# Kernel tuning notes

Hardware: AMD Instinct MI355X
Metric: run time of the kernel (lower is better)

Reference implementation:

```python
import math
import jax, jax.numpy as jnp
import numpy as np

V, D, L, H, B, T = 50257, 1024, 6, 16, 4, 1024
HD = D // H  # 64


def layer_norm(x, s, b, eps=1e-5):
    m = jnp.mean(x, axis=-1, keepdims=True)
    v = jnp.var(x, axis=-1, keepdims=True)
    return (x - m) * jax.lax.rsqrt(v + eps) * s + b


def setup_inputs() -> dict:
    key = jax.random.key(0)
    ks = jax.random.split(key, 8)
    sc = 0.02
    return {
        "input_ids": jax.random.randint(ks[0], (B, T), 0, V),
        "attention_mask": jnp.ones((B, T), jnp.float32),
        "pool_mask": jax.random.uniform(ks[1], (B, T), dtype=jnp.float32),
        "embed": jax.random.normal(ks[2], (V, D), jnp.float32) * sc,
        "ln1_s": jnp.ones((L, D), jnp.float32),
        "ln1_b": jnp.zeros((L, D), jnp.float32),
        "qkv_w": jax.random.normal(ks[3], (L, D, 3 * D), jnp.float32) * sc,
        "qkv_b": jnp.zeros((L, 3 * D), jnp.float32),
        "attn_w": jax.random.normal(ks[4], (L, D, D), jnp.float32) * sc,
        "attn_b": jnp.zeros((L, D), jnp.float32),
        "ln2_s": jnp.ones((L, D), jnp.float32),
        "ln2_b": jnp.zeros((L, D), jnp.float32),
        "fc1_w": jax.random.normal(ks[5], (L, D, 4 * D), jnp.float32) * sc,
        "fc1_b": jnp.zeros((L, 4 * D), jnp.float32),
        "fc2_w": jax.random.normal(ks[6], (L, 4 * D, D), jnp.float32) * sc,
        "fc2_b": jnp.zeros((L, D), jnp.float32),
    }


def reference(input_ids, attention_mask, pool_mask, embed, ln1_s, ln1_b,
              qkv_w, qkv_b, attn_w, attn_b, ln2_s, ln2_b,
              fc1_w, fc1_b, fc2_w, fc2_b):
    h = embed[input_ids]  # [B,T,D]
    # key_mask.clamp(min=0) then log(clamp(min=1e-9)) == log(clip(mask, 1e-9))
    log_mask = jnp.log(jnp.clip(attention_mask, 1e-9))[:, None, None, :]  # [B,1,1,T]
    scale = 1.0 / math.sqrt(HD)

    def block(h, p):
        l1s, l1b, qw, qb, aw, ab, l2s, l2b, f1w, f1b, f2w, f2b = p
        x = layer_norm(h, l1s, l1b)
        qkv = jnp.einsum('btd,de->bte', x, qw) + qb          # [B,T,3D]
        qkv = qkv.reshape(B, T, H, 3 * HD).transpose(0, 2, 1, 3)  # [B,H,T,3hd]
        q, k, v = jnp.split(qkv, 3, axis=-1)
        scores = jnp.einsum('bhqd,bhkd->bhqk', q, k) * scale + log_mask
        probs = jax.nn.softmax(scores, axis=-1)
        ctx = jnp.einsum('bhqk,bhkd->bhqd', probs, v)
        ctx = ctx.transpose(0, 2, 1, 3).reshape(B, T, D)
        h = h + jnp.einsum('btd,de->bte', ctx, aw) + ab
        y = layer_norm(h, l2s, l2b)
        y = jax.nn.gelu(jnp.einsum('btd,df->btf', y, f1w) + f1b, approximate=False)
        h = h + jnp.einsum('btf,fd->btd', y, f2w) + f2b
        # NOTE: source applies post_attention_layernorm a second time at block end
        h = layer_norm(h, l2s, l2b)
        return h, None

    params = (ln1_s, ln1_b, qkv_w, qkv_b, attn_w, attn_b,
              ln2_s, ln2_b, fc1_w, fc1_b, fc2_w, fc2_b)
    h, _ = jax.lax.scan(block, h, params)

    # pool with pool_mask, then L2-normalize (F.normalize, eps=1e-12)
    m = pool_mask[..., None]
    sent = (h * m).sum(axis=1) / jnp.clip(m.sum(axis=1), 1e-6)
    return sent / jnp.clip(jnp.linalg.norm(sent, axis=-1, keepdims=True), 1e-12)
```

## Files before the change

kernel.cpp:

```cpp
#include <hip/hip_runtime.h>
#include <hip/hip_bf16.h>
#include <math.h>

#define VV 50257
#define DD 1024
#define LL 6
#define HH 16
#define BB 4
#define TT 1024
#define HD 64
#define BT (BB*TT)

typedef __attribute__((ext_vector_type(8))) short bf16x8;
typedef __attribute__((ext_vector_type(8))) _Float16 f16x8;
typedef __attribute__((ext_vector_type(4))) short short4v;
typedef __attribute__((ext_vector_type(4))) float f32x4;
typedef __attribute__((ext_vector_type(16))) float f32x16;

__device__ inline float b2f(unsigned short u) {
    unsigned x = ((unsigned)u) << 16;
    return __uint_as_float(x);
}
__device__ inline unsigned short f2b(float f) {
    __hip_bfloat16 h = __float2bfloat16(f);
    return *reinterpret_cast<unsigned short*>(&h);
}
__device__ inline void plswap32(unsigned &dst, unsigned &src) {
    asm("v_permlane32_swap_b32 %0, %1" : "+v"(dst), "+v"(src));
}

#define GLOAD16(g, l) __builtin_amdgcn_global_load_lds( \
    (const __attribute__((address_space(1))) void*)(g), \
    (__attribute__((address_space(3))) void*)(l), 16, 0, 0)

__launch_bounds__(256)
__global__ void gather_embed(const int* __restrict__ ids, const float* __restrict__ emb,
                             float* __restrict__ h) {
    const int row = blockIdx.x;
    const int id = ids[row];
    const float4* src = (const float4*)(emb + (size_t)id * DD);
    float4* dst = (float4*)(h + (size_t)row * DD);
    dst[threadIdx.x] = src[threadIdx.x];
}

__launch_bounds__(256)
__global__ void logmask_k(const float* __restrict__ am, float* __restrict__ lm) {
    int i = blockIdx.x * 256 + threadIdx.x;
    if (i < BT) lm[i] = logf(fmaxf(am[i], 1e-9f));
}

__device__ inline float block_sum_256(float v, float* ws) {
    #pragma unroll
    for (int o = 32; o > 0; o >>= 1) v += __shfl_down(v, o);
    const int lane = threadIdx.x & 63, wid = threadIdx.x >> 6;
    if (lane == 0) ws[wid] = v;
    __syncthreads();
    return ws[0] + ws[1] + ws[2] + ws[3];
}

__launch_bounds__(256)
__global__ void ln_f32(const float* __restrict__ in, float* __restrict__ out,
                       const float* __restrict__ g, const float* __restrict__ bta) {
    __shared__ float ws1[4], ws2[4];
    const int row = blockIdx.x, tid = threadIdx.x;
    const float* x = in + (size_t)row * DD;
    float4 v = *(const float4*)(x + tid * 4);
    float s = v.x + v.y + v.z + v.w;
    float tot = block_sum_256(s, ws1);
    float m = tot * (1.0f / 1024.0f);
    float d0 = v.x - m, d1 = v.y - m, d2 = v.z - m, d3 = v.w - m;
    float s2 = d0*d0 + d1*d1 + d2*d2 + d3*d3;
    float tot2 = block_sum_256(s2, ws2);
    float rstd = rsqrtf(tot2 * (1.0f / 1024.0f) + 1e-5f);
    const int d = tid * 4;
    float4 gg = *(const float4*)(g + d);
    float4 bb = *(const float4*)(bta + d);
    float4 o;
    o.x = d0 * rstd * gg.x + bb.x;
    o.y = d1 * rstd * gg.y + bb.y;
    o.z = d2 * rstd * gg.z + bb.z;
    o.w = d3 * rstd * gg.w + bb.w;
    *(float4*)(out + (size_t)row * DD + d) = o;
}

__launch_bounds__(256)
__global__ void ln_bf16(const float* __restrict__ in, unsigned short* __restrict__ out,
                        const float* __restrict__ g, const float* __restrict__ bta) {
    __shared__ float ws1[4], ws2[4];
    const int row = blockIdx.x, tid = threadIdx.x;
    const float* x = in + (size_t)row * DD;
    float4 v = *(const float4*)(x + tid * 4);
    float s = v.x + v.y + v.z + v.w;
    float tot = block_sum_256(s, ws1);
    float m = tot * (1.0f / 1024.0f);
    float d0 = v.x - m, d1 = v.y - m, d2 = v.z - m, d3 = v.w - m;
    float s2 = d0*d0 + d1*d1 + d2*d2 + d3*d3;
    float tot2 = block_sum_256(s2, ws2);
    float rstd = rsqrtf(tot2 * (1.0f / 1024.0f) + 1e-5f);
    const int d = tid * 4;
    float4 gg = *(const float4*)(g + d);
    float4 bb = *(const float4*)(bta + d);
    ushort4 o;
    o.x = f2b(d0 * rstd * gg.x + bb.x);
    o.y = f2b(d1 * rstd * gg.y + bb.y);
    o.z = f2b(d2 * rstd * gg.z + bb.z);
    o.w = f2b(d3 * rstd * gg.w + bb.w);
    *(ushort4*)(out + (size_t)row * DD + d) = o;
}

__launch_bounds__(256)
__global__ void wtrans(const float* __restrict__ W, unsigned short* __restrict__ Wt,
                       int K, int N) {
    __shared__ float tile[64][65];
    const int k0 = blockIdx.y * 64, n0 = blockIdx.x * 64;
    const int lrow = threadIdx.x >> 4;
    const int lcol = (threadIdx.x & 15) * 4;
    #pragma unroll
    for (int i = 0; i < 4; ++i) {
        const int r = lrow + i * 16;
        *(float4*)&tile[r][lcol] = *(const float4*)(W + (size_t)(k0 + r) * N + n0 + lcol);
    }
    __syncthreads();
    #pragma unroll
    for (int i = 0; i < 4; ++i) {
        const int n = lrow + i * 16;
        ushort4 o;
        o.x = f2b(tile[lcol + 0][n]);
        o.y = f2b(tile[lcol + 1][n]);
        o.z = f2b(tile[lcol + 2][n]);
        o.w = f2b(tile[lcol + 3][n]);
        *(ushort4*)(Wt + (size_t)(n0 + n) * K + k0 + lcol) = o;
    }
}

#define BM 128
#define BN 128
#define BK 64

__device__ inline float gelu_f(float v) {
    return 0.5f * v * (1.0f + erff(v * 0.70710678118654752f));
}

template<int EPI>
__launch_bounds__(256)
__global__ void gemm_mfma(const unsigned short* __restrict__ A,
                          const unsigned short* __restrict__ Bt,
                          const float* __restrict__ bias, void* __restrict__ Cv,
                          int M, int K, int N) {
    __shared__ short As[BM * BK];
    __shared__ short Bs[BN * BK];

    const int tid = threadIdx.x;
    const int wid = tid >> 6, lane = tid & 63;

    const int nwg = gridDim.x * gridDim.y;
    int bid = blockIdx.y * gridDim.x + blockIdx.x;
    bid = (bid & 7) * (nwg >> 3) + (bid >> 3);
    const int m0 = (bid / gridDim.x) * BM;
    const int n0 = (bid % gridDim.x) * BN;

    const int wr = wid >> 1, wc = wid & 1;
    const int fr = lane & 15, fq = lane >> 4;

    const int rowS = tid >> 3;
    const int cS = tid & 7;
    const int coff = (cS ^ (rowS & 7)) * 8;
    const unsigned short* aS = A  + (size_t)(m0 + rowS) * K + coff;
    const unsigned short* bS = Bt + (size_t)(n0 + rowS) * K + coff;
    const size_t rstride = (size_t)32 * K;

    const int key = fr & 7;
    const int c0 = fq ^ key;
    int aoff[4], boff[4];
    #pragma unroll
    for (int m = 0; m < 4; ++m) aoff[m] = (wr * 64 + m * 16 + fr) * BK + c0 * 8;
    #pragma unroll
    for (int n = 0; n < 4; ++n) boff[n] = (wc * 64 + n * 16 + fr) * BK + c0 * 8;

    f32x4 acc[4][4];
    #pragma unroll
    for (int m = 0; m < 4; ++m)
        #pragma unroll
        for (int n = 0; n < 4; ++n) acc[m][n] = (f32x4){0.f, 0.f, 0.f, 0.f};

    for (int kk = 0; kk < K; kk += BK) {
        __syncthreads();
        #pragma unroll
        for (int r = 0; r < 4; ++r) {
            GLOAD16(aS + kk + r * rstride, &As[(wid * 64 + r * 256) * 8]);
            GLOAD16(bS + kk + r * rstride, &Bs[(wid * 64 + r * 256) * 8]);
        }
        __syncthreads();
        #pragma unroll
        for (int s = 0; s < 2; ++s) {
            bf16x8 af[4], bfr[4];
            #pragma unroll
            for (int m = 0; m < 4; ++m) af[m] = *(const bf16x8*)&As[aoff[m] ^ (s << 5)];
            #pragma unroll
            for (int n = 0; n < 4; ++n) bfr[n] = *(const bf16x8*)&Bs[boff[n] ^ (s << 5)];
            #pragma unroll
            for (int m = 0; m < 4; ++m)
                #pragma unroll
                for (int n = 0; n < 4; ++n)
                    acc[m][n] = __builtin_amdgcn_mfma_f32_16x16x32_bf16(
                        af[m], bfr[n], acc[m][n], 0, 0, 0);
        }
    }

    float bias_v[4];
    #pragma unroll
    for (int n = 0; n < 4; ++n) bias_v[n] = bias[n0 + wc * 64 + n * 16 + fr];

    #pragma unroll
    for (int m = 0; m < 4; ++m) {
        #pragma unroll
        for (int n = 0; n < 4; ++n) {
            const int col = n0 + wc * 64 + n * 16 + fr;
            #pragma unroll
            for (int j = 0; j < 4; ++j) {
                const int row = m0 + wr * 64 + m * 16 + fq * 4 + j;
                float v = acc[m][n][j] + bias_v[n];
                if (EPI == 1) {
                    float* C = (float*)Cv;
                    C[(size_t)row * N + col] += v;
                } else {
                    if (EPI == 2) v = gelu_f(v);
                    unsigned short* C = (unsigned short*)Cv;
                    C[(size_t)row * N + col] = f2b(v);
                }
            }
        }
    }
}

__launch_bounds__(256)
__global__ void attn_mfma(const unsigned short* __restrict__ qkv,
                          const float* __restrict__ lm,
                          unsigned short* __restrict__ ctx) {
    int bid = blockIdx.x;
    const int ww = (bid & 7) * 64 + (bid >> 3);
    const int bh = ww >> 3, qt = ww & 7;
    const int b = bh >> 4, hh = bh & 15;
    const int tid = threadIdx.x, w = tid >> 6, lane = tid & 63;
    const int lo = lane & 31, hf = lane >> 5;
    const int q_row = qt * 128 + w * 32 + lo;

    __shared__ short Ks[32 * 64];
    __shared__ short Vt[64 * 40];
    __shared__ float lms[32];

    bf16x8 qf[4];
    {
        const unsigned short* qbase = qkv + (size_t)(b * TT + q_row) * 3072 + hh * 192;
        #pragma unroll
        for (int kk = 0; kk < 4; ++kk)
            qf[kk] = *(const bf16x8*)(qbase + (2 * kk + hf) * 8);
    }

    const int skey = tid >> 3, sc = tid & 7;
    const unsigned short* kptr = qkv + (size_t)(b * TT + skey) * 3072 + hh * 192 + 64
                                 + ((sc ^ (skey & 7)) * 8);
    short* kdst = &Ks[w * 64 * 8];

    const int vkey = tid & 31, vc = tid >> 5;
    const unsigned short* vptr = qkv + (size_t)(b * TT + vkey) * 3072 + hh * 192 + 128 + vc * 8;

    f32x16 o0, o1;
    #pragma unroll
    for (int j = 0; j < 16; ++j) { o0[j] = 0.f; o1[j] = 0.f; }
    float M = -1e30f, S = 0.f;

    for (int kt = 0; kt < 32; ++kt) {
        __syncthreads();
        GLOAD16(kptr, kdst);
        bf16x8 vv = *(const bf16x8*)vptr;
        if (tid < 32) lms[tid] = lm[b * TT + kt * 32 + tid];
        #pragma unroll
        for (int i = 0; i < 8; ++i) {
            _Float16 hv = (_Float16)b2f((unsigned short)vv[i]);
            Vt[(vc * 8 + i) * 40 + vkey] = *reinterpret_cast<short*>(&hv);
        }
        kptr += (size_t)32 * 3072;
        vptr += (size_t)32 * 3072;
        __syncthreads();

        f32x16 s16;
        #pragma unroll
        for (int j = 0; j < 16; ++j) s16[j] = 0.f;
        __builtin_amdgcn_s_setprio(1);
        #pragma unroll
        for (int kk = 0; kk < 4; ++kk) {
            const int c = (2 * kk + hf) ^ (lo & 7);
            bf16x8 kf = *(const bf16x8*)&Ks[lo * 64 + c * 8];
            s16 = __builtin_amdgcn_mfma_f32_32x32x16_bf16(kf, qf[kk], s16, 0, 0, 0);
        }
        __builtin_amdgcn_s_setprio(0);

        float p[16];
        float mx = -1e30f;
        #pragma unroll
        for (int j = 0; j < 16; ++j) {
            const int kidx = (j & 3) + 8 * (j >> 2) + 4 * hf;
            float sv = s16[j] * 0.125f + lms[kidx];
            p[j] = sv;
            mx = fmaxf(mx, sv);
        }
        mx = fmaxf(mx, __shfl_xor(mx, 32));
        if (!__all(mx <= M + 8.0f)) {
            const float Mn = fmaxf(M, mx);
            const float f = __expf(M - Mn);
            S *= f;
            #pragma unroll
            for (int j = 0; j < 16; ++j) { o0[j] *= f; o1[j] *= f; }
            M = Mn;
        }

        unsigned short ph[16];
        float ls = 0.f;
        #pragma unroll
        for (int j = 0; j < 16; ++j) {
            _Float16 hq = (_Float16)__expf(p[j] - M);
            ph[j] = *reinterpret_cast<unsigned short*>(&hq);
            ls += (float)hq;
        }
        ls += __shfl_xor(ls, 32);
        S += ls;

        unsigned ra = (unsigned)ph[0]  | ((unsigned)ph[1]  << 16);
        unsigned rb = (unsigned)ph[2]  | ((unsigned)ph[3]  << 16);
        unsigned rc = (unsigned)ph[4]  | ((unsigned)ph[5]  << 16);
        unsigned rd = (unsigned)ph[6]  | ((unsigned)ph[7]  << 16);
        unsigned re = (unsigned)ph[8]  | ((unsigned)ph[9]  << 16);
        unsigned rf = (unsigned)ph[10] | ((unsigned)ph[11] << 16);
        unsigned rg = (unsigned)ph[12] | ((unsigned)ph[13] << 16);
        unsigned rh = (unsigned)ph[14] | ((unsigned)ph[15] << 16);
        plswap32(ra, rc);
        plswap32(rb, rd);
        plswap32(re, rg);
        plswap32(rf, rh);
        union { unsigned u[4]; f16x8 v; } p1, p2;
        p1.u[0] = ra; p1.u[1] = rb; p1.u[2] = rc; p1.u[3] = rd;
        p2.u[0] = re; p2.u[1] = rf; p2.u[2] = rg; p2.u[3] = rh;

        f16x8 va0 = *(const f16x8*)&Vt[lo * 40 + hf * 8];
        f16x8 va1 = *(const f16x8*)&Vt[lo * 40 + 16 + hf * 8];
        f16x8 vb0 = *(const f16x8*)&Vt[(32 + lo) * 40 + hf * 8];
        f16x8 vb1 = *(const f16x8*)&Vt[(32 + lo) * 40 + 16 + hf * 8];
        __builtin_amdgcn_s_setprio(1);
        o0 = __builtin_amdgcn_mfma_f32_32x32x16_f16(va0, p1.v, o0, 0, 0, 0);
        o0 = __builtin_amdgcn_mfma_f32_32x32x16_f16(va1, p2.v, o0, 0, 0, 0);
        o1 = __builtin_amdgcn_mfma_f32_32x32x16_f16(vb0, p1.v, o1, 0, 0, 0);
        o1 = __builtin_amdgcn_mfma_f32_32x32x16_f16(vb1, p2.v, o1, 0, 0, 0);
        __builtin_amdgcn_s_setprio(0);
    }

    const float inv = 1.f / S;
    unsigned short* obase = ctx + (size_t)(b * TT + q_row) * DD + hh * 64;
    #pragma unroll
    for (int g = 0; g < 4; ++g) {
        const int dbase = 8 * g + 4 * hf;
        ushort4 w0, w1;
        w0.x = f2b(o0[4*g+0] * inv); w0.y = f2b(o0[4*g+1] * inv);
        w0.z = f2b(o0[4*g+2] * inv); w0.w = f2b(o0[4*g+3] * inv);
        w1.x = f2b(o1[4*g+0] * inv); w1.y = f2b(o1[4*g+1] * inv);
        w1.z = f2b(o1[4*g+2] * inv); w1.w = f2b(o1[4*g+3] * inv);
        *(ushort4*)(obase + dbase) = w0;
        *(ushort4*)(obase + 32 + dbase) = w1;
    }
}

__launch_bounds__(256)
__global__ void pool_partial(const float* __restrict__ h, const float* __restrict__ pm,
                             float* __restrict__ part) {
    const int b = blockIdx.x >> 4, c = blockIdx.x & 15;
    const int tid = threadIdx.x;
    const float* hp = h + (size_t)(b * TT + c * 64) * DD + tid * 4;
    const float* pp = pm + b * TT + c * 64;
    float4 acc = {0.f, 0.f, 0.f, 0.f};
    for (int t = 0; t < 64; ++t) {
        const float p = pp[t];
        float4 v = *(const float4*)(hp + (size_t)t * DD);
        acc.x += p * v.x; acc.y += p * v.y; acc.z += p * v.z; acc.w += p * v.w;
    }
    *(float4*)(part + (size_t)blockIdx.x * DD + tid * 4) = acc;
}

__launch_bounds__(1024)
__global__ void pool_final(const float* __restrict__ part, const float* __restrict__ pm,
                           float* __restrict__ out) {
    const int b = blockIdx.x, d = threadIdx.x;
    __shared__ float ws[16];
    float s = pm[b * TT + d];
    #pragma unroll
    for (int o = 32; o > 0; o >>= 1) s += __shfl_down(s, o);
    if ((d & 63) == 0) ws[d >> 6] = s;
    __syncthreads();
    float msum = 0.f;
    #pragma unroll
    for (int i = 0; i < 16; ++i) msum += ws[i];

    float acc = 0.f;
    #pragma unroll
    for (int c = 0; c < 16; ++c)
        acc += part[(size_t)(b * 16 + c) * DD + d];
    const float sent = acc / fmaxf(msum, 1e-6f);

    float qv = sent * sent;
    #pragma unroll
    for (int o = 32; o > 0; o >>= 1) qv += __shfl_down(qv, o);
    __syncthreads();
    if ((d & 63) == 0) ws[d >> 6] = qv;
    __syncthreads();
    float nrm = 0.f;
    #pragma unroll
    for (int i = 0; i < 16; ++i) nrm += ws[i];
    nrm = sqrtf(nrm);
    out[b * DD + d] = sent / fmaxf(nrm, 1e-12f);
}

extern "C" void kernel_launch(void* const* d_in, const int* in_sizes, int n_in,
                              void* d_out, int out_size, void* d_ws, size_t ws_size,
                              hipStream_t stream) {
    const int*   ids    = (const int*)  d_in[0];
    const float* amask  = (const float*)d_in[1];
    const float* pmask  = (const float*)d_in[2];
    const float* embed  = (const float*)d_in[3];
    const float* ln1_s  = (const float*)d_in[4];
    const float* ln1_b  = (const float*)d_in[5];
    const float* qkv_w  = (const float*)d_in[6];
    const float* qkv_b  = (const float*)d_in[7];
    const float* attn_w = (const float*)d_in[8];
    const float* attn_b = (const float*)d_in[9];
    const float* ln2_s  = (const float*)d_in[10];
    const float* ln2_b  = (const float*)d_in[11];
    const float* fc1_w  = (const float*)d_in[12];
    const float* fc1_b  = (const float*)d_in[13];
    const float* fc2_w  = (const float*)d_in[14];
    const float* fc2_b  = (const float*)d_in[15];

    char* wp = (char*)d_ws;
    float* h = (float*)wp;                 wp += (size_t)BT * DD * 4;
    unsigned short* qkv_bf = (unsigned short*)wp; wp += (size_t)BT * 3072 * 2;
    unsigned short* act_bf = (unsigned short*)wp; wp += (size_t)BT * 4096 * 2;
    unsigned short* x_bf   = (unsigned short*)wp; wp += (size_t)BT * DD * 2;
    unsigned short* wq_t   = (unsigned short*)wp; wp += (size_t)3072 * 1024 * 2;
    unsigned short* wa_t   = (unsigned short*)wp; wp += (size_t)1024 * 1024 * 2;
    unsigned short* w1_t   = (unsigned short*)wp; wp += (size_t)4096 * 1024 * 2;
    unsigned short* w2_t   = (unsigned short*)wp; wp += (size_t)1024 * 4096 * 2;
    float* lm = (float*)wp;                wp += (size_t)BT * 4;
    float* part = (float*)wp;              wp += (size_t)64 * DD * 4;

    gather_embed<<<BT, 256, 0, stream>>>(ids, embed, h);
    logmask_k<<<16, 256, 0, stream>>>(amask, lm);

    for (int l = 0; l < LL; ++l) {
        const size_t lD = (size_t)l * DD;

        wtrans<<<dim3(3072/64, 1024/64), 256, 0, stream>>>(
            qkv_w + (size_t)l * 1024 * 3072, wq_t, 1024, 3072);
        wtrans<<<dim3(1024/64, 1024/64), 256, 0, stream>>>(
            attn_w + (size_t)l * 1024 * 1024, wa_t, 1024, 1024);
        wtrans<<<dim3(4096/64, 1024/64), 256, 0, stream>>>(
            fc1_w + (size_t)l * 1024 * 4096, w1_t, 1024, 4096);
        wtrans<<<dim3(1024/64, 4096/64), 256, 0, stream>>>(
            fc2_w + (size_t)l * 4096 * 1024, w2_t, 4096, 1024);

        ln_bf16<<<BT, 256, 0, stream>>>(h, x_bf, ln1_s + lD, ln1_b + lD);
        gemm_mfma<0><<<dim3(3072/BN, BT/BM), 256, 0, stream>>>(
            x_bf, wq_t, qkv_b + (size_t)l * 3072, qkv_bf, BT, 1024, 3072);
        attn_mfma<<<512, 256, 0, stream>>>(qkv_bf, lm, x_bf);
        gemm_mfma<1><<<dim3(1024/BN, BT/BM), 256, 0, stream>>>(
            x_bf, wa_t, attn_b + lD, h, BT, 1024, 1024);
        ln_bf16<<<BT, 256, 0, stream>>>(h, x_bf, ln2_s + lD, ln2_b + lD);
        gemm_mfma<2><<<dim3(4096/BN, BT/BM), 256, 0, stream>>>(
            x_bf, w1_t, fc1_b + (size_t)l * 4096, act_bf, BT, 1024, 4096);
        gemm_mfma<1><<<dim3(1024/BN, BT/BM), 256, 0, stream>>>(
            act_bf, w2_t, fc2_b + lD, h, BT, 4096, 1024);
        ln_f32<<<BT, 256, 0, stream>>>(h, h, ln2_s + lD, ln2_b + lD);
    }

    pool_partial<<<64, 256, 0, stream>>>(h, pmask, part);
    pool_final<<<BB, 1024, 0, stream>>>(part, pmask, (float*)d_out);
}
```

Before: 1.870 ms.

## Fuse layernorms and weight transposes, narrow N-tiles, double-buffer attention K/V

Fuses the end-of-block layernorm with the next layer's first layernorm into one kernel, and merges the four weight-transpose launches into a single launch. The GEMM is templated on N-fragments so the N=1024 GEMMs use 64-wide tiles and launch more workgroups. The attention kernel now processes 64-key tiles with double-buffered K/V in shared memory, loading the next tile while computing the current one. These changes target launch overhead, low occupancy on the narrow GEMMs, and load latency in attention, at the cost of more shared memory per attention block and more code.

```diff
diff --git a/kernel.cpp b/kernel.cpp
--- a/kernel.cpp
+++ b/kernel.cpp
@@ -13,7 +13,6 @@
 
 typedef __attribute__((ext_vector_type(8))) short bf16x8;
 typedef __attribute__((ext_vector_type(8))) _Float16 f16x8;
-typedef __attribute__((ext_vector_type(4))) short short4v;
 typedef __attribute__((ext_vector_type(4))) float f32x4;
 typedef __attribute__((ext_vector_type(16))) float f32x16;
 
@@ -109,10 +108,55 @@
 }
 
 __launch_bounds__(256)
-__global__ void wtrans(const float* __restrict__ W, unsigned short* __restrict__ Wt,
-                       int K, int N) {
+__global__ void ln_dual(const float* __restrict__ in, float* __restrict__ outf,
+                        const float* __restrict__ g2, const float* __restrict__ b2v,
+                        unsigned short* __restrict__ outb,
+                        const float* __restrict__ g1, const float* __restrict__ b1v) {
+    __shared__ float ws1[4], ws2[4], ws3[4], ws4[4];
+    const int row = blockIdx.x, tid = threadIdx.x;
+    const int d = tid * 4;
+    float4 v = *(const float4*)(in + (size_t)row * DD + d);
+    float s = v.x + v.y + v.z + v.w;
+    float m = block_sum_256(s, ws1) * (1.0f / 1024.0f);
+    float d0 = v.x - m, d1 = v.y - m, d2 = v.z - m, d3 = v.w - m;
+    float s2 = d0*d0 + d1*d1 + d2*d2 + d3*d3;
+    float rstd = rsqrtf(block_sum_256(s2, ws2) * (1.0f / 1024.0f) + 1e-5f);
+    float4 gg = *(const float4*)(g2 + d);
+    float4 bb = *(const float4*)(b2v + d);
+    float4 y;
+    y.x = d0 * rstd * gg.x + bb.x;
+    y.y = d1 * rstd * gg.y + bb.y;
+    y.z = d2 * rstd * gg.z + bb.z;
+    y.w = d3 * rstd * gg.w + bb.w;
+    *(float4*)(outf + (size_t)row * DD + d) = y;
+    float t = y.x + y.y + y.z + y.w;
+    float m2 = block_sum_256(t, ws3) * (1.0f / 1024.0f);
+    float e0 = y.x - m2, e1 = y.y - m2, e2 = y.z - m2, e3 = y.w - m2;
+    float t2 = e0*e0 + e1*e1 + e2*e2 + e3*e3;
+    float rstd2 = rsqrtf(block_sum_256(t2, ws4) * (1.0f / 1024.0f) + 1e-5f);
+    float4 g1v = *(const float4*)(g1 + d);
+    float4 b1x = *(const float4*)(b1v + d);
+    ushort4 o;
+    o.x = f2b(e0 * rstd2 * g1v.x + b1x.x);
+    o.y = f2b(e1 * rstd2 * g1v.y + b1x.y);
+    o.z = f2b(e2 * rstd2 * g1v.z + b1x.z);
+    o.w = f2b(e3 * rstd2 * g1v.w + b1x.w);
+    *(ushort4*)(outb + (size_t)row * DD + d) = o;
+}
+
+__launch_bounds__(256)
+__global__ void wtrans4(const float* __restrict__ wq, unsigned short* __restrict__ wqo,
+                        const float* __restrict__ wa, unsigned short* __restrict__ wao,
+                        const float* __restrict__ w1, unsigned short* __restrict__ w1o,
+                        const float* __restrict__ w2, unsigned short* __restrict__ w2o) {
     __shared__ float tile[64][65];
-    const int k0 = blockIdx.y * 64, n0 = blockIdx.x * 64;
+    int id = blockIdx.x;
+    const float* W; unsigned short* Wt; int K, N, tx, ty;
+    if (id < 768)       { W = wq; Wt = wqo; K = 1024; N = 3072; tx = id % 48; ty = id / 48; }
+    else if (id < 1024) { id -= 768;  W = wa; Wt = wao; K = 1024; N = 1024; tx = id & 15; ty = id >> 4; }
+    else if (id < 2048) { id -= 1024; W = w1; Wt = w1o; K = 1024; N = 4096; tx = id & 63; ty = id >> 6; }
+    else                { id -= 2048; W = w2; Wt = w2o; K = 4096; N = 1024; tx = id & 15; ty = id >> 4; }
+    const int k0 = ty * 64, n0 = tx * 64;
     const int lrow = threadIdx.x >> 4;
     const int lcol = (threadIdx.x & 15) * 4;
     #pragma unroll
@@ -134,19 +178,19 @@
 }
 
 #define BM 128
-#define BN 128
 #define BK 64
 
 __device__ inline float gelu_f(float v) {
     return 0.5f * v * (1.0f + erff(v * 0.70710678118654752f));
 }
 
-template<int EPI>
+template<int EPI, int NFRAG>
 __launch_bounds__(256)
 __global__ void gemm_mfma(const unsigned short* __restrict__ A,
                           const unsigned short* __restrict__ Bt,
                           const float* __restrict__ bias, void* __restrict__ Cv,
                           int M, int K, int N) {
+    constexpr int BN = NFRAG * 32;
     __shared__ short As[BM * BK];
     __shared__ short Bs[BN * BK];
 
@@ -171,51 +215,52 @@
 
     const int key = fr & 7;
     const int c0 = fq ^ key;
-    int aoff[4], boff[4];
+    int aoff[4], boff[NFRAG];
     #pragma unroll
     for (int m = 0; m < 4; ++m) aoff[m] = (wr * 64 + m * 16 + fr) * BK + c0 * 8;
     #pragma unroll
-    for (int n = 0; n < 4; ++n) boff[n] = (wc * 64 + n * 16 + fr) * BK + c0 * 8;
-
-    f32x4 acc[4][4];
+    for (int n = 0; n < NFRAG; ++n) boff[n] = (wc * (NFRAG * 16) + n * 16 + fr) * BK + c0 * 8;
+
+    f32x4 acc[4][NFRAG];
     #pragma unroll
     for (int m = 0; m < 4; ++m)
         #pragma unroll
-        for (int n = 0; n < 4; ++n) acc[m][n] = (f32x4){0.f, 0.f, 0.f, 0.f};
+        for (int n = 0; n < NFRAG; ++n) acc[m][n] = (f32x4){0.f, 0.f, 0.f, 0.f};
 
     for (int kk = 0; kk < K; kk += BK) {
         __syncthreads();
         #pragma unroll
-        for (int r = 0; r < 4; ++r) {
+        for (int r = 0; r < 4; ++r)
             GLOAD16(aS + kk + r * rstride, &As[(wid * 64 + r * 256) * 8]);
+        #pragma unroll
+        for (int r = 0; r < NFRAG; ++r)
             GLOAD16(bS + kk + r * rstride, &Bs[(wid * 64 + r * 256) * 8]);
-        }
         __syncthreads();
         #pragma unroll
         for (int s = 0; s < 2; ++s) {
-            bf16x8 af[4], bfr[4];
+            bf16x8 af[4], bfr[NFRAG];
             #pragma unroll
             for (int m = 0; m < 4; ++m) af[m] = *(const bf16x8*)&As[aoff[m] ^ (s << 5)];
             #pragma unroll
-            for (int n = 0; n < 4; ++n) bfr[n] = *(const bf16x8*)&Bs[boff[n] ^ (s << 5)];
+            for (int n = 0; n < NFRAG; ++n) bfr[n] = *(const bf16x8*)&Bs[boff[n] ^ (s << 5)];
             #pragma unroll
             for (int m = 0; m < 4; ++m)
                 #pragma unroll
-                for (int n = 0; n < 4; ++n)
+                for (int n = 0; n < NFRAG; ++n)
                     acc[m][n] = __builtin_amdgcn_mfma_f32_16x16x32_bf16(
                         af[m], bfr[n], acc[m][n], 0, 0, 0);
         }
     }
 
-    float bias_v[4];
-    #pragma unroll
-    for (int n = 0; n < 4; ++n) bias_v[n] = bias[n0 + wc * 64 + n * 16 + fr];
+    float bias_v[NFRAG];
+    #pragma unroll
+    for (int n = 0; n < NFRAG; ++n) bias_v[n] = bias[n0 + wc * (NFRAG * 16) + n * 16 + fr];
 
     #pragma unroll
     for (int m = 0; m < 4; ++m) {
         #pragma unroll
-        for (int n = 0; n < 4; ++n) {
-            const int col = n0 + wc * 64 + n * 16 + fr;
+        for (int n = 0; n < NFRAG; ++n) {
+            const int col = n0 + wc * (NFRAG * 16) + n * 16 + fr;
             #pragma unroll
             for (int j = 0; j < 4; ++j) {
                 const int row = m0 + wr * 64 + m * 16 + fq * 4 + j;
@@ -245,9 +290,9 @@
     const int lo = lane & 31, hf = lane >> 5;
     const int q_row = qt * 128 + w * 32 + lo;
 
-    __shared__ short Ks[32 * 64];
-    __shared__ short Vt[64 * 40];
-    __shared__ float lms[32];
+    __shared__ short Ks[2][64 * 64];
+    __shared__ short Vt[2][64 * 72];
+    __shared__ float lms[2][64];
 
     bf16x8 qf[4];
     {
@@ -257,101 +302,125 @@
             qf[kk] = *(const bf16x8*)(qbase + (2 * kk + hf) * 8);
     }
 
-    const int skey = tid >> 3, sc = tid & 7;
-    const unsigned short* kptr = qkv + (size_t)(b * TT + skey) * 3072 + hh * 192 + 64
-                                 + ((sc ^ (skey & 7)) * 8);
-    short* kdst = &Ks[w * 64 * 8];
-
+    const int r0 = tid >> 3, cS = tid & 7;
+    const unsigned short* kp = qkv + (size_t)(b * TT + r0) * 3072 + hh * 192 + 64
+                               + ((cS ^ (r0 & 7)) * 8);
     const int vkey = tid & 31, vc = tid >> 5;
-    const unsigned short* vptr = qkv + (size_t)(b * TT + vkey) * 3072 + hh * 192 + 128 + vc * 8;
+    const unsigned short* vp = qkv + (size_t)(b * TT + vkey) * 3072 + hh * 192 + 128 + vc * 8;
+    const float* lmrow = lm + b * TT;
 
     f32x16 o0, o1;
     #pragma unroll
     for (int j = 0; j < 16; ++j) { o0[j] = 0.f; o1[j] = 0.f; }
     float M = -1e30f, S = 0.f;
 
-    for (int kt = 0; kt < 32; ++kt) {
+    {
+        GLOAD16(kp, &Ks[0][(w * 64) * 8]);
+        GLOAD16(kp + (size_t)32 * 3072, &Ks[0][(256 + w * 64) * 8]);
+        bf16x8 v0 = *(const bf16x8*)vp;
+        bf16x8 v1 = *(const bf16x8*)(vp + (size_t)32 * 3072);
+        if (tid < 64) lms[0][tid] = lmrow[tid];
+        #pragma unroll
+        for (int i = 0; i < 8; ++i) {
+            _Float16 h0 = (_Float16)b2f((unsigned short)v0[i]);
+            _Float16 h1 = (_Float16)b2f((unsigned short)v1[i]);
+            Vt[0][(vc * 8 + i) * 72 + vkey] = *reinterpret_cast<short*>(&h0);
+            Vt[0][(vc * 8 + i) * 72 + 32 + vkey] = *reinterpret_cast<short*>(&h1);
+        }
+    }
+
+    int cur = 0;
+    for (int kt = 0; kt < 16; ++kt) {
         __syncthreads();
-        GLOAD16(kptr, kdst);
-        bf16x8 vv = *(const bf16x8*)vptr;
-        if (tid < 32) lms[tid] = lm[b * TT + kt * 32 + tid];
-        #pragma unroll
-        for (int i = 0; i < 8; ++i) {
-            _Float16 hv = (_Float16)b2f((unsigned short)vv[i]);
-            Vt[(vc * 8 + i) * 40 + vkey] = *reinterpret_cast<short*>(&hv);
+        if (kt < 15) {
+            const int nb = cur ^ 1;
+            const size_t off = (size_t)((kt + 1) * 64) * 3072;
+            GLOAD16(kp + off, &Ks[nb][(w * 64) * 8]);
+            GLOAD16(kp + off + (size_t)32 * 3072, &Ks[nb][(256 + w * 64) * 8]);
+            bf16x8 v0 = *(const bf16x8*)(vp + off);
+            bf16x8 v1 = *(const bf16x8*)(vp + off + (size_t)32 * 3072);
+            if (tid < 64) lms[nb][tid] = lmrow[(kt + 1) * 64 + tid];
+            #pragma unroll
+            for (int i = 0; i < 8; ++i) {
+                _Float16 h0 = (_Float16)b2f((unsigned short)v0[i]);
+                _Float16 h1 = (_Float16)b2f((unsigned short)v1[i]);
+                Vt[nb][(vc * 8 + i) * 72 + vkey] = *reinterpret_cast<short*>(&h0);
+                Vt[nb][(vc * 8 + i) * 72 + 32 + vkey] = *reinterpret_cast<short*>(&h1);
+            }
         }
-        kptr += (size_t)32 * 3072;
-        vptr += (size_t)32 * 3072;
-        __syncthreads();
-
-        f32x16 s16;
-        #pragma unroll
-        for (int j = 0; j < 16; ++j) s16[j] = 0.f;
-        __builtin_amdgcn_s_setprio(1);
-        #pragma unroll
-        for (int kk = 0; kk < 4; ++kk) {
-            const int c = (2 * kk + hf) ^ (lo & 7);
-            bf16x8 kf = *(const bf16x8*)&Ks[lo * 64 + c * 8];
-            s16 = __builtin_amdgcn_mfma_f32_32x32x16_bf16(kf, qf[kk], s16, 0, 0, 0);
+
+        #pragma unroll
+        for (int g = 0; g < 2; ++g) {
+            f32x16 s16;
+            #pragma unroll
+            for (int j = 0; j < 16; ++j) s16[j] = 0.f;
+            __builtin_amdgcn_s_setprio(1);
+            #pragma unroll
+            for (int kk = 0; kk < 4; ++kk) {
+                const int c = (2 * kk + hf) ^ (lo & 7);
+                bf16x8 kf = *(const bf16x8*)&Ks[cur][((g * 32 + lo) * 8 + c) * 8];
+                s16 = __builtin_amdgcn_mfma_f32_32x32x16_bf16(kf, qf[kk], s16, 0, 0, 0);
+            }
+            __builtin_amdgcn_s_setprio(0);
+
+            float p[16];
+            float mx = -1e30f;
+            #pragma unroll
+            for (int j = 0; j < 16; ++j) {
+                const int kidx = g * 32 + (j & 3) + 8 * (j >> 2) + 4 * hf;
+                float sv = s16[j] * 0.125f + lms[cur][kidx];
+                p[j] = sv;
+                mx = fmaxf(mx, sv);
+            }
+            mx = fmaxf(mx, __shfl_xor(mx, 32));
+            if (!__all(mx <= M + 8.0f)) {
+                const float Mn = fmaxf(M, mx);
+                const float f = __expf(M - Mn);
+                S *= f;
+                #pragma unroll
+                for (int j = 0; j < 16; ++j) { o0[j] *= f; o1[j] *= f; }
+                M = Mn;
+            }
+
+            unsigned short ph[16];
+            float ls = 0.f;
+            #pragma unroll
+            for (int j = 0; j < 16; ++j) {
+                _Float16 hq = (_Float16)__expf(p[j] - M);
+                ph[j] = *reinterpret_cast<unsigned short*>(&hq);
+                ls += (float)hq;
+            }
+            ls += __shfl_xor(ls, 32);
+            S += ls;
+
+            unsigned ra = (unsigned)ph[0]  | ((unsigned)ph[1]  << 16);
+            unsigned rb = (unsigned)ph[2]  | ((unsigned)ph[3]  << 16);
+            unsigned rc = (unsigned)ph[4]  | ((unsigned)ph[5]  << 16);
+            unsigned rd = (unsigned)ph[6]  | ((unsigned)ph[7]  << 16);
+            unsigned re = (unsigned)ph[8]  | ((unsigned)ph[9]  << 16);
+            unsigned rf = (unsigned)ph[10] | ((unsigned)ph[11] << 16);
+            unsigned rg = (unsigned)ph[12] | ((unsigned)ph[13] << 16);
+            unsigned rh = (unsigned)ph[14] | ((unsigned)ph[15] << 16);
+            plswap32(ra, rc);
+            plswap32(rb, rd);
+            plswap32(re, rg);
+            plswap32(rf, rh);
+            union { unsigned u[4]; f16x8 v; } p1, p2;
+            p1.u[0] = ra; p1.u[1] = rb; p1.u[2] = rc; p1.u[3] = rd;
+            p2.u[0] = re; p2.u[1] = rf; p2.u[2] = rg; p2.u[3] = rh;
+
+            f16x8 va0 = *(const f16x8*)&Vt[cur][lo * 72 + g * 32 + hf * 8];
+            f16x8 va1 = *(const f16x8*)&Vt[cur][lo * 72 + g * 32 + 16 + hf * 8];
+            f16x8 vb0 = *(const f16x8*)&Vt[cur][(32 + lo) * 72 + g * 32 + hf * 8];
+            f16x8 vb1 = *(const f16x8*)&Vt[cur][(32 + lo) * 72 + g * 32 + 16 + hf * 8];
+            __builtin_amdgcn_s_setprio(1);
+            o0 = __builtin_amdgcn_mfma_f32_32x32x16_f16(va0, p1.v, o0, 0, 0, 0);
+            o0 = __builtin_amdgcn_mfma_f32_32x32x16_f16(va1, p2.v, o0, 0, 0, 0);
+            o1 = __builtin_amdgcn_mfma_f32_32x32x16_f16(vb0, p1.v, o1, 0, 0, 0);
+            o1 = __builtin_amdgcn_mfma_f32_32x32x16_f16(vb1, p2.v, o1, 0, 0, 0);
+            __builtin_amdgcn_s_setprio(0);
         }
-        __builtin_amdgcn_s_setprio(0);
-
-        float p[16];
-        float mx = -1e30f;
-        #pragma unroll
-        for (int j = 0; j < 16; ++j) {
-            const int kidx = (j & 3) + 8 * (j >> 2) + 4 * hf;
-            float sv = s16[j] * 0.125f + lms[kidx];
-            p[j] = sv;
-            mx = fmaxf(mx, sv);
-        }
-        mx = fmaxf(mx, __shfl_xor(mx, 32));
-        if (!__all(mx <= M + 8.0f)) {
-            const float Mn = fmaxf(M, mx);
-            const float f = __expf(M - Mn);
-            S *= f;
-            #pragma unroll
-            for (int j = 0; j < 16; ++j) { o0[j] *= f; o1[j] *= f; }
-            M = Mn;
-        }
-
-        unsigned short ph[16];
-        float ls = 0.f;
-        #pragma unroll
-        for (int j = 0; j < 16; ++j) {
-            _Float16 hq = (_Float16)__expf(p[j] - M);
-            ph[j] = *reinterpret_cast<unsigned short*>(&hq);
-            ls += (float)hq;
-        }
-        ls += __shfl_xor(ls, 32);
-        S += ls;
-
-        unsigned ra = (unsigned)ph[0]  | ((unsigned)ph[1]  << 16);
-        unsigned rb = (unsigned)ph[2]  | ((unsigned)ph[3]  << 16);
-        unsigned rc = (unsigned)ph[4]  | ((unsigned)ph[5]  << 16);
-        unsigned rd = (unsigned)ph[6]  | ((unsigned)ph[7]  << 16);
-        unsigned re = (unsigned)ph[8]  | ((unsigned)ph[9]  << 16);
-        unsigned rf = (unsigned)ph[10] | ((unsigned)ph[11] << 16);
-        unsigned rg = (unsigned)ph[12] | ((unsigned)ph[13] << 16);
-        unsigned rh = (unsigned)ph[14] | ((unsigned)ph[15] << 16);
-        plswap32(ra, rc);
-        plswap32(rb, rd);
-        plswap32(re, rg);
-        plswap32(rf, rh);
-        union { unsigned u[4]; f16x8 v; } p1, p2;
-        p1.u[0] = ra; p1.u[1] = rb; p1.u[2] = rc; p1.u[3] = rd;
-        p2.u[0] = re; p2.u[1] = rf; p2.u[2] = rg; p2.u[3] = rh;
-
-        f16x8 va0 = *(const f16x8*)&Vt[lo * 40 + hf * 8];
-        f16x8 va1 = *(const f16x8*)&Vt[lo * 40 + 16 + hf * 8];
-        f16x8 vb0 = *(const f16x8*)&Vt[(32 + lo) * 40 + hf * 8];
-        f16x8 vb1 = *(const f16x8*)&Vt[(32 + lo) * 40 + 16 + hf * 8];
-        __builtin_amdgcn_s_setprio(1);
-        o0 = __builtin_amdgcn_mfma_f32_32x32x16_f16(va0, p1.v, o0, 0, 0, 0);
-        o0 = __builtin_amdgcn_mfma_f32_32x32x16_f16(va1, p2.v, o0, 0, 0, 0);
-        o1 = __builtin_amdgcn_mfma_f32_32x32x16_f16(vb0, p1.v, o1, 0, 0, 0);
-        o1 = __builtin_amdgcn_mfma_f32_32x32x16_f16(vb1, p2.v, o1, 0, 0, 0);
-        __builtin_amdgcn_s_setprio(0);
+        cur ^= 1;
     }
 
     const float inv = 1.f / S;
@@ -452,31 +521,34 @@
 
     gather_embed<<<BT, 256, 0, stream>>>(ids, embed, h);
     logmask_k<<<16, 256, 0, stream>>>(amask, lm);
+    ln_bf16<<<BT, 256, 0, stream>>>(h, x_bf, ln1_s, ln1_b);
 
     for (int l = 0; l < LL; ++l) {
         const size_t lD = (size_t)l * DD;
 
-        wtrans<<<dim3(3072/64, 1024/64), 256, 0, stream>>>(
-            qkv_w + (size_t)l * 1024 * 3072, wq_t, 1024, 3072);
-        wtrans<<<dim3(1024/64, 1024/64), 256, 0, stream>>>(
-            attn_w + (size_t)l * 1024 * 1024, wa_t, 1024, 1024);
-        wtrans<<<dim3(4096/64, 1024/64), 256, 0, stream>>>(
-            fc1_w + (size_t)l * 1024 * 4096, w1_t, 1024, 4096);
-        wtrans<<<dim3(1024/64, 4096/64), 256, 0, stream>>>(
-            fc2_w + (size_t)l * 4096 * 1024, w2_t, 4096, 1024);
-
-        ln_bf16<<<BT, 256, 0, stream>>>(h, x_bf, ln1_s + lD, ln1_b + lD);
-        gemm_mfma<0><<<dim3(3072/BN, BT/BM), 256, 0, stream>>>(
+        wtrans4<<<3072, 256, 0, stream>>>(
+            qkv_w + (size_t)l * 1024 * 3072, wq_t,
+            attn_w + (size_t)l * 1024 * 1024, wa_t,
+            fc1_w + (size_t)l * 1024 * 4096, w1_t,
+            fc2_w + (size_t)l * 4096 * 1024, w2_t);
+
+        gemm_mfma<0, 4><<<dim3(3072/128, BT/BM), 256, 0, stream>>>(
             x_bf, wq_t, qkv_b + (size_t)l * 3072, qkv_bf, BT, 1024, 3072);
         attn_mfma<<<512, 256, 0, stream>>>(qkv_bf, lm, x_bf);
-        gemm_mfma<1><<<dim3(1024/BN, BT/BM), 256, 0, stream>>>(
+        gemm_mfma<1, 2><<<dim3(1024/64, BT/BM), 256, 0, stream>>>(
             x_bf, wa_t, attn_b + lD, h, BT, 1024, 1024);
         ln_bf16<<<BT, 256, 0, stream>>>(h, x_bf, ln2_s + lD, ln2_b + lD);
-        gemm_mfma<2><<<dim3(4096/BN, BT/BM), 256, 0, stream>>>(
+        gemm_mfma<2, 4><<<dim3(4096/128, BT/BM), 256, 0, stream>>>(
             x_bf, w1_t, fc1_b + (size_t)l * 4096, act_bf, BT, 1024, 4096);
-        gemm_mfma<1><<<dim3(1024/BN, BT/BM), 256, 0, stream>>>(
+        gemm_mfma<1, 2><<<dim3(1024/64, BT/BM), 256, 0, stream>>>(
             act_bf, w2_t, fc2_b + lD, h, BT, 4096, 1024);
-        ln_f32<<<BT, 256, 0, stream>>>(h, h, ln2_s + lD, ln2_b + lD);
+
+        if (l < LL - 1) {
+            ln_dual<<<BT, 256, 0, stream>>>(h, h, ln2_s + lD, ln2_b + lD,
+                                            x_bf, ln1_s + lD + DD, ln1_b + lD + DD);
+        } else {
+            ln_f32<<<BT, 256, 0, stream>>>(h, h, ln2_s + lD, ln2_b + lD);
+        }
     }
 
     pool_partial<<<64, 256, 0, stream>>>(h, pmask, part);
```

New measurement: 1.630 ms. 12.8% less time.
